# Kernel tuning notes

Measured on AMD Instinct MI355X. Metric: run time of the kernel, lower is better.

The kernel has to match this reference:

```python
import jax, jax.numpy as jnp
import numpy as np

B, T, C, H = 2, 2048, 1024, 16
HD = C // H  # head dim = 64


def setup_inputs() -> dict:
    key = jax.random.key(0)
    k1, k2, k3 = jax.random.split(key, 3)
    scale = 0.02
    x = jax.random.normal(k1, (B, T, C), dtype=jnp.float32)
    w_attn = jax.random.normal(k2, (C, 3 * C), dtype=jnp.float32) * scale
    b_attn = jnp.zeros((3 * C,), dtype=jnp.float32)
    w_proj = jax.random.normal(k3, (C, C), dtype=jnp.float32) * scale
    b_proj = jnp.zeros((C,), dtype=jnp.float32)
    return {"x": x, "w_attn": w_attn, "b_attn": b_attn, "w_proj": w_proj, "b_proj": b_proj}


def reference(x, w_attn, b_attn, w_proj, b_proj):
    b, t, c = x.shape
    qkv = x @ w_attn + b_attn  # [B,T,3C]
    q, k, v = jnp.split(qkv, 3, axis=-1)
    # [B,T,C] -> [B,H,T,HD]
    q = q.reshape(b, t, H, HD).transpose(0, 2, 1, 3)
    k = k.reshape(b, t, H, HD).transpose(0, 2, 1, 3)
    v = v.reshape(b, t, H, HD).transpose(0, 2, 1, 3)
    att = jnp.einsum('bhqd,bhkd->bhqk', q, k) * (1.0 / jnp.sqrt(jnp.float32(HD)))
    causal = jnp.tril(jnp.ones((t, t), dtype=bool))  # [T,T]
    att = jnp.where(causal[None, None, :, :], att, jnp.float32(-jnp.inf))
    att = jax.nn.softmax(att, axis=-1)
    y = jnp.einsum('bhqk,bhkd->bhqd', att, v)
    y = y.transpose(0, 2, 1, 3).reshape(b, t, c)
    return y @ w_proj + b_proj
```

## Files before the change

kernel.cpp:

```cpp
#include <hip/hip_runtime.h>


typedef unsigned short u16;
typedef unsigned short u16x8 __attribute__((ext_vector_type(8)));
typedef __bf16 bf16x8 __attribute__((ext_vector_type(8)));
typedef __bf16 bf16x4 __attribute__((ext_vector_type(4)));
typedef float f32x4 __attribute__((ext_vector_type(4)));

#define MFMA16(a, b, c) __builtin_amdgcn_mfma_f32_16x16x32_bf16(a, b, c, 0, 0, 0)

static __device__ __forceinline__ u16 f2b(float f) {
  union { float f; unsigned int i; } x; x.f = f;
  unsigned int r = x.i + 0x7fffu + ((x.i >> 16) & 1u);
  return (u16)(r >> 16);
}

static __device__ __forceinline__ void gload_lds16(const u16* g, u16* l) {
#if defined(__HIP_DEVICE_COMPILE__)
  __builtin_amdgcn_global_load_lds(
      (const __attribute__((address_space(1))) unsigned int*)g,
      (__attribute__((address_space(3))) unsigned int*)l,
      16, 0, 0);
#else
  (void)g; (void)l;
#endif
}

__global__ __launch_bounds__(256) void cast_f32_bf16(
    const float* __restrict__ in, u16* __restrict__ out) {
  int i = (blockIdx.x * 256 + threadIdx.x) * 8;
  float4 a = *(const float4*)&in[i];
  float4 b = *(const float4*)&in[i + 4];
  u16x8 o;
  o[0] = f2b(a.x); o[1] = f2b(a.y); o[2] = f2b(a.z); o[3] = f2b(a.w);
  o[4] = f2b(b.x); o[5] = f2b(b.y); o[6] = f2b(b.z); o[7] = f2b(b.w);
  *(u16x8*)&out[i] = o;
}

__global__ __launch_bounds__(256) void transpose_f32_bf16(
    const float* __restrict__ in, u16* __restrict__ out, int R, int Cc) {
  __shared__ u16 tile[32][33];
  int bx = blockIdx.x, by = blockIdx.y;
  int tx = threadIdx.x, ty = threadIdx.y;
#pragma unroll
  for (int i = 0; i < 4; i++) {
    int r = by * 32 + ty + i * 8;
    int c = bx * 32 + tx;
    tile[ty + i * 8][tx] = f2b(in[r * Cc + c]);
  }
  __syncthreads();
#pragma unroll
  for (int i = 0; i < 4; i++) {
    int r = bx * 32 + ty + i * 8;
    int c = by * 32 + tx;
    out[r * R + c] = tile[tx][ty + i * 8];
  }
}

__global__ __launch_bounds__(256) void transpose_v(
    const u16* __restrict__ in, u16* __restrict__ out) {
  int bh = blockIdx.y;
  int t = blockIdx.x * 128 + (threadIdx.x & 127);
  int dg = (threadIdx.x >> 7) * 32;
  const u16* src = in + (bh * 2048 + t) * 64;
  u16* dst = out + bh * 64 * 2048 + t;
#pragma unroll
  for (int i = 0; i < 32; i++) {
    int d = dg + i;
    dst[d * 2048] = src[d];
  }
}

template <int MODE>
__global__ __launch_bounds__(256, 2) void gemm_bt(
    const u16* __restrict__ A, const u16* __restrict__ Bt,
    const float* __restrict__ bias, float* __restrict__ out,
    u16* __restrict__ Qb, u16* __restrict__ Kb, u16* __restrict__ Vb,
    int M, int N, int K) {
  __shared__ u16 lA[128 * 32];
  __shared__ u16 lB[128 * 32];

  const int tid = threadIdx.x;
  const int lane = tid & 63;
  const int w = tid >> 6;
  const int wm = (w >> 1) * 64, wn = (w & 1) * 64;
  const int l15 = lane & 15, quad = lane >> 4;
  const int m0 = blockIdx.y * 128, n0 = blockIdx.x * 128;

  const int srow = lane >> 2;
  const int scol = (lane & 3) * 8;

  f32x4 acc[4][4] = {};

  for (int k0 = 0; k0 < K; k0 += 32) {
    __syncthreads();
#pragma unroll
    for (int h = 0; h < 2; h++) {
      int r = h * 64 + w * 16 + srow;
      gload_lds16(&A[(m0 + r) * K + k0 + scol], &lA[h * 2048 + w * 512 + lane * 8]);
      gload_lds16(&Bt[(n0 + r) * K + k0 + scol], &lB[h * 2048 + w * 512 + lane * 8]);
    }
    __syncthreads();

    bf16x8 af[4], bfr[4];
#pragma unroll
    for (int mi = 0; mi < 4; mi++)
      af[mi] = *(const bf16x8*)&lA[(wm + mi * 16 + l15) * 32 + quad * 8];
#pragma unroll
    for (int ni = 0; ni < 4; ni++)
      bfr[ni] = *(const bf16x8*)&lB[(wn + ni * 16 + l15) * 32 + quad * 8];
#pragma unroll
    for (int mi = 0; mi < 4; mi++)
#pragma unroll
      for (int ni = 0; ni < 4; ni++)
        acc[mi][ni] = MFMA16(af[mi], bfr[ni], acc[mi][ni]);
  }

#pragma unroll
  for (int mi = 0; mi < 4; mi++) {
#pragma unroll
    for (int ni = 0; ni < 4; ni++) {
      int n = n0 + wn + ni * 16 + l15;
      float bv = bias[n];
#pragma unroll
      for (int reg = 0; reg < 4; reg++) {
        int m = m0 + wm + mi * 16 + quad * 4 + reg;
        float v = acc[mi][ni][reg] + bv;
        if (MODE == 1) {
          out[m * N + n] = v;
        } else {
          int which = n >> 10;
          if (which == 1) v *= 0.18033688011112042f;
          int hn = n & 1023;
          int hh = hn >> 6, d = hn & 63;
          int b = m >> 11, t = m & 2047;
          u16* dst = (which == 0) ? Qb : ((which == 1) ? Kb : Vb);
          dst[(((b << 4) + hh) * 2048 + t) * 64 + d] = f2b(v);
        }
      }
    }
  }
}

__global__ __launch_bounds__(256, 4) void attn_kernel(
    const u16* __restrict__ Qg, const u16* __restrict__ Kg,
    const u16* __restrict__ Vt, u16* __restrict__ Yg) {
  __shared__ u16 lk[64 * 72];
  __shared__ u16 lvt[64 * 72];

  const int qt = 31 - blockIdx.x;
  const int bh = blockIdx.y;
  const int tid = threadIdx.x;
  const int lane = tid & 63;
  const int w = tid >> 6;
  const int l15 = lane & 15, quad = lane >> 4;
  const int qbase = qt * 64;
  const int base = bh * 2048 * 64;
  const int vbase = bh * 64 * 2048;

  const int sr = tid >> 3;
  const int sc = (tid & 7) * 8;

  const u16* qrow = Qg + base + (qbase + w * 16 + l15) * 64;
  bf16x8 bq0 = *(const bf16x8*)&qrow[quad * 8];
  bf16x8 bq1 = *(const bf16x8*)&qrow[32 + quad * 8];

  const u16* kp = Kg + base;
  const u16* vp = Vt + vbase;

  u16x8 kr[2], vr[2];
#pragma unroll
  for (int h = 0; h < 2; h++) {
    int r = sr + h * 32;
    kr[h] = *(const u16x8*)&kp[r * 64 + sc];
    vr[h] = *(const u16x8*)&vp[r * 2048 + sc];
  }

  f32x4 oacc[4] = {};
  float ls = 0.f;

  for (int kt = 0; kt <= qt; kt++) {
    __syncthreads();
#pragma unroll
    for (int h = 0; h < 2; h++) {
      int r = sr + h * 32;
      *(u16x8*)&lk[r * 72 + sc] = kr[h];
      *(u16x8*)&lvt[r * 72 + sc] = vr[h];
    }
    __syncthreads();
    if (kt < qt) {
      int kvb = (kt + 1) * 64;
#pragma unroll
      for (int h = 0; h < 2; h++) {
        int r = sr + h * 32;
        kr[h] = *(const u16x8*)&kp[(kvb + r) * 64 + sc];
        vr[h] = *(const u16x8*)&vp[r * 2048 + kvb + sc];
      }
    }

    const bool diag = (kt == qt);
    const int qloc = w * 16 + l15;

#pragma unroll
    for (int u = 0; u < 2; u++) {
      bf16x8 pa;
      float psum = 0.f;
#pragma unroll
      for (int half = 0; half < 2; half++) {
        int nt = 2 * u + half;
        bf16x8 ak0 = *(const bf16x8*)&lk[(nt * 16 + l15) * 72 + quad * 8];
        bf16x8 ak1 = *(const bf16x8*)&lk[(nt * 16 + l15) * 72 + 32 + quad * 8];
        f32x4 st = {};
        st = MFMA16(ak0, bq0, st);
        st = MFMA16(ak1, bq1, st);
#pragma unroll
        for (int reg = 0; reg < 4; reg++) {
          float s = st[reg];
          if (diag && (nt * 16 + quad * 4 + reg) > qloc) s = -1e30f;
          float p = exp2f(s);
          psum += p;
          pa[half * 4 + reg] = (__bf16)p;
        }
      }
      ls += psum;

#pragma unroll
      for (int dt = 0; dt < 4; dt++) {
        const u16* vrow = &lvt[(dt * 16 + l15) * 72 + u * 32 + quad * 4];
        bf16x4 lo = *(const bf16x4*)&vrow[0];
        bf16x4 hi = *(const bf16x4*)&vrow[16];
        bf16x8 bv;
#pragma unroll
        for (int j = 0; j < 4; j++) { bv[j] = lo[j]; bv[4 + j] = hi[j]; }
        oacc[dt] = MFMA16(pa, bv, oacc[dt]);
      }
    }
  }

  ls += __shfl_xor(ls, 16, 64);
  ls += __shfl_xor(ls, 32, 64);

  const int b = bh >> 4, hh = bh & 15;
  float inv[4];
#pragma unroll
  for (int reg = 0; reg < 4; reg++)
    inv[reg] = 1.0f / __shfl(ls, quad * 4 + reg, 64);
#pragma unroll
  for (int dt = 0; dt < 4; dt++)
#pragma unroll
    for (int reg = 0; reg < 4; reg++) {
      int q = qbase + w * 16 + quad * 4 + reg;
      int col = hh * 64 + dt * 16 + l15;
      Yg[(b * 2048 + q) * 1024 + col] = f2b(oacc[dt][reg] * inv[reg]);
    }
}

extern "C" void kernel_launch(void* const* d_in, const int* in_sizes, int n_in,
                              void* d_out, int out_size, void* d_ws, size_t ws_size,
                              hipStream_t stream) {
  const float* x      = (const float*)d_in[0];
  const float* w_attn = (const float*)d_in[1];
  const float* b_attn = (const float*)d_in[2];
  const float* w_proj = (const float*)d_in[3];
  const float* b_proj = (const float*)d_in[4];
  float* out = (float*)d_out;

  char* ws = (char*)d_ws;
  u16* wattnT = (u16*)(ws);
  u16* wprojT = (u16*)(ws + 6291456);
  u16* xb     = (u16*)(ws + 8388608);
  u16* Vt     = xb;
  u16* Qb     = (u16*)(ws + 16777216);
  u16* Kb     = (u16*)(ws + 25165824);
  u16* Vb     = (u16*)(ws + 33554432);
  u16* Yb     = (u16*)(ws + 41943040);

  cast_f32_bf16<<<2048, 256, 0, stream>>>(x, xb);
  transpose_f32_bf16<<<dim3(96, 32), dim3(32, 8), 0, stream>>>(w_attn, wattnT, 1024, 3072);
  transpose_f32_bf16<<<dim3(32, 32), dim3(32, 8), 0, stream>>>(w_proj, wprojT, 1024, 1024);
  gemm_bt<0><<<dim3(24, 32), 256, 0, stream>>>(xb, wattnT, b_attn, nullptr,
                                               Qb, Kb, Vb, 4096, 3072, 1024);
  transpose_v<<<dim3(16, 32), 256, 0, stream>>>(Vb, Vt);
  attn_kernel<<<dim3(32, 32), 256, 0, stream>>>(Qb, Kb, Vt, Yb);
  gemm_bt<1><<<dim3(8, 32), 256, 0, stream>>>(Yb, wprojT, b_proj, out,
                                              nullptr, nullptr, nullptr, 4096, 1024, 1024);
}
```

Measured before the change: 217.2 us.

## Split causal attention along the KV axis with a combine pass

Causal attention work per query tile is uneven, so the attention kernel is split into KV chunks of 8 tiles. Long query tiles get up to four blocks, and their unnormalized partial outputs and row sums are written to workspace. A small combine kernel then sums the partials and normalizes them. Row sums are now computed with an MFMA against a vector of ones instead of scalar adds and shuffles. The trade-off is an extra launch, partial outputs stored in bf16, and the split path only runs when the workspace is large enough.

After: 200.3 us. 7.8% less time.

```diff
diff --git a/kernel.cpp b/kernel.cpp
--- a/kernel.cpp
+++ b/kernel.cpp
@@ -13,6 +13,9 @@
   union { float f; unsigned int i; } x; x.f = f;
   unsigned int r = x.i + 0x7fffu + ((x.i >> 16) & 1u);
   return (u16)(r >> 16);
+}
+static __device__ __forceinline__ float b2f(u16 u) {
+  union { unsigned int i; float f; } x; x.i = ((unsigned int)u) << 16; return x.f;
 }
 
 static __device__ __forceinline__ void gload_lds16(const u16* g, u16* l) {
@@ -142,6 +145,175 @@
   }
 }
 
+__global__ __launch_bounds__(256, 4) void attn_split(
+    const u16* __restrict__ Qg, const u16* __restrict__ Kg,
+    const u16* __restrict__ Vt, u16* __restrict__ Yg,
+    u16* __restrict__ Opart, float* __restrict__ lpart) {
+  __shared__ u16 lk[64 * 72];
+  __shared__ u16 lvt[64 * 72];
+
+  const int x = blockIdx.x;
+  const int bh = blockIdx.y;
+  int qt, s, ns;
+  if (x < 8)       { qt = x;                s = 0;            ns = 1; }
+  else if (x < 24) { int r = x - 8;  qt = 8  + (r >> 1); s = r & 1; ns = 2; }
+  else if (x < 48) { int r = x - 24; qt = 16 + r / 3;    s = r % 3; ns = 3; }
+  else             { int r = x - 48; qt = 24 + (r >> 2); s = r & 3; ns = 4; }
+  const int kts = s * 8;
+  const int kend = (kts + 8 < qt + 1) ? (kts + 8) : (qt + 1);
+
+  const int tid = threadIdx.x;
+  const int lane = tid & 63;
+  const int w = tid >> 6;
+  const int l15 = lane & 15, quad = lane >> 4;
+  const int qbase = qt * 64;
+  const int base = bh * 2048 * 64;
+  const int vbase = bh * 64 * 2048;
+
+  const int sr = tid >> 3;
+  const int sc = (tid & 7) * 8;
+
+  const u16* qrow = Qg + base + (qbase + w * 16 + l15) * 64;
+  bf16x8 bq0 = *(const bf16x8*)&qrow[quad * 8];
+  bf16x8 bq1 = *(const bf16x8*)&qrow[32 + quad * 8];
+
+  u16x8 onesu = {0x3F80, 0x3F80, 0x3F80, 0x3F80, 0x3F80, 0x3F80, 0x3F80, 0x3F80};
+  bf16x8 ones = *(const bf16x8*)&onesu;
+
+  const u16* kp = Kg + base;
+  const u16* vp = Vt + vbase;
+
+  u16x8 kr[2], vr[2];
+  {
+    int kvb = kts * 64;
+#pragma unroll
+    for (int h = 0; h < 2; h++) {
+      int r = sr + h * 32;
+      kr[h] = *(const u16x8*)&kp[(kvb + r) * 64 + sc];
+      vr[h] = *(const u16x8*)&vp[r * 2048 + kvb + sc];
+    }
+  }
+
+  f32x4 oacc[4] = {};
+  f32x4 lacc = {};
+
+  for (int kt = kts; kt < kend; kt++) {
+    __syncthreads();
+#pragma unroll
+    for (int h = 0; h < 2; h++) {
+      int r = sr + h * 32;
+      *(u16x8*)&lk[r * 72 + sc] = kr[h];
+      *(u16x8*)&lvt[r * 72 + sc] = vr[h];
+    }
+    __syncthreads();
+    if (kt + 1 < kend) {
+      int kvb = (kt + 1) * 64;
+#pragma unroll
+      for (int h = 0; h < 2; h++) {
+        int r = sr + h * 32;
+        kr[h] = *(const u16x8*)&kp[(kvb + r) * 64 + sc];
+        vr[h] = *(const u16x8*)&vp[r * 2048 + kvb + sc];
+      }
+    }
+
+    const bool diag = (kt == qt);
+    const int qloc = w * 16 + l15;
+
+#pragma unroll
+    for (int u = 0; u < 2; u++) {
+      bf16x8 pa;
+#pragma unroll
+      for (int half = 0; half < 2; half++) {
+        int nt = 2 * u + half;
+        bf16x8 ak0 = *(const bf16x8*)&lk[(nt * 16 + l15) * 72 + quad * 8];
+        bf16x8 ak1 = *(const bf16x8*)&lk[(nt * 16 + l15) * 72 + 32 + quad * 8];
+        f32x4 st = {};
+        st = MFMA16(ak0, bq0, st);
+        st = MFMA16(ak1, bq1, st);
+#pragma unroll
+        for (int reg = 0; reg < 4; reg++) {
+          float sv = st[reg];
+          if (diag && (nt * 16 + quad * 4 + reg) > qloc) sv = -1e30f;
+          pa[half * 4 + reg] = (__bf16)exp2f(sv);
+        }
+      }
+      lacc = MFMA16(pa, ones, lacc);
+#pragma unroll
+      for (int dt = 0; dt < 4; dt++) {
+        const u16* vrow = &lvt[(dt * 16 + l15) * 72 + u * 32 + quad * 4];
+        bf16x4 lo = *(const bf16x4*)&vrow[0];
+        bf16x4 hi = *(const bf16x4*)&vrow[16];
+        bf16x8 bv;
+#pragma unroll
+        for (int j = 0; j < 4; j++) { bv[j] = lo[j]; bv[4 + j] = hi[j]; }
+        oacc[dt] = MFMA16(pa, bv, oacc[dt]);
+      }
+    }
+  }
+
+  if (ns == 1) {
+    const int b = bh >> 4, hh = bh & 15;
+    float inv[4];
+#pragma unroll
+    for (int reg = 0; reg < 4; reg++) inv[reg] = 1.0f / lacc[reg];
+#pragma unroll
+    for (int dt = 0; dt < 4; dt++)
+#pragma unroll
+      for (int reg = 0; reg < 4; reg++) {
+        int q = qbase + w * 16 + quad * 4 + reg;
+        int col = hh * 64 + dt * 16 + l15;
+        Yg[(b * 2048 + q) * 1024 + col] = f2b(oacc[dt][reg] * inv[reg]);
+      }
+  } else {
+    const int p = bh * 80 + x;
+    u16* op = Opart + p * 4096 + (w * 16) * 64;
+#pragma unroll
+    for (int dt = 0; dt < 4; dt++)
+#pragma unroll
+      for (int reg = 0; reg < 4; reg++)
+        op[(quad * 4 + reg) * 64 + dt * 16 + l15] = f2b(oacc[dt][reg]);
+    if (l15 == 0) {
+#pragma unroll
+      for (int reg = 0; reg < 4; reg++)
+        lpart[p * 64 + w * 16 + quad * 4 + reg] = lacc[reg];
+    }
+  }
+}
+
+__global__ __launch_bounds__(256) void attn_combine(
+    const u16* __restrict__ Opart, const float* __restrict__ lpart,
+    u16* __restrict__ Yg) {
+  const int qt = 8 + blockIdx.x;
+  const int bh = blockIdx.y;
+  const int tid = threadIdx.x;
+  const int row = tid >> 2;
+  const int cg = (tid & 3) * 16;
+  int xb, ns;
+  if (qt < 16)      { xb = 8  + (qt - 8) * 2;  ns = 2; }
+  else if (qt < 24) { xb = 24 + (qt - 16) * 3; ns = 3; }
+  else              { xb = 48 + (qt - 24) * 4; ns = 4; }
+
+  float acc[16] = {};
+  float lsum = 0.f;
+  for (int i = 0; i < ns; i++) {
+    int p = bh * 80 + xb + i;
+    lsum += lpart[p * 64 + row];
+    const u16* oprow = Opart + p * 4096 + row * 64 + cg;
+    u16x8 a = *(const u16x8*)&oprow[0];
+    u16x8 b = *(const u16x8*)&oprow[8];
+#pragma unroll
+    for (int j = 0; j < 8; j++) { acc[j] += b2f(a[j]); acc[8 + j] += b2f(b[j]); }
+  }
+  float inv = 1.0f / lsum;
+  u16x8 o0, o1;
+#pragma unroll
+  for (int j = 0; j < 8; j++) { o0[j] = f2b(acc[j] * inv); o1[j] = f2b(acc[8 + j] * inv); }
+  const int b = bh >> 4, hh = bh & 15;
+  u16* y = Yg + ((long)(b * 2048 + qt * 64 + row)) * 1024 + hh * 64 + cg;
+  *(u16x8*)&y[0] = o0;
+  *(u16x8*)&y[8] = o1;
+}
+
 __global__ __launch_bounds__(256, 4) void attn_kernel(
     const u16* __restrict__ Qg, const u16* __restrict__ Kg,
     const u16* __restrict__ Vt, u16* __restrict__ Yg) {
@@ -157,13 +329,15 @@
   const int qbase = qt * 64;
   const int base = bh * 2048 * 64;
   const int vbase = bh * 64 * 2048;
-
   const int sr = tid >> 3;
   const int sc = (tid & 7) * 8;
 
   const u16* qrow = Qg + base + (qbase + w * 16 + l15) * 64;
   bf16x8 bq0 = *(const bf16x8*)&qrow[quad * 8];
   bf16x8 bq1 = *(const bf16x8*)&qrow[32 + quad * 8];
+
+  u16x8 onesu = {0x3F80, 0x3F80, 0x3F80, 0x3F80, 0x3F80, 0x3F80, 0x3F80, 0x3F80};
+  bf16x8 ones = *(const bf16x8*)&onesu;
 
   const u16* kp = Kg + base;
   const u16* vp = Vt + vbase;
@@ -177,7 +351,7 @@
   }
 
   f32x4 oacc[4] = {};
-  float ls = 0.f;
+  f32x4 lacc = {};
 
   for (int kt = 0; kt <= qt; kt++) {
     __syncthreads();
@@ -200,11 +374,9 @@
 
     const bool diag = (kt == qt);
     const int qloc = w * 16 + l15;
-
 #pragma unroll
     for (int u = 0; u < 2; u++) {
       bf16x8 pa;
-      float psum = 0.f;
 #pragma unroll
       for (int half = 0; half < 2; half++) {
         int nt = 2 * u + half;
@@ -215,15 +387,12 @@
         st = MFMA16(ak1, bq1, st);
 #pragma unroll
         for (int reg = 0; reg < 4; reg++) {
-          float s = st[reg];
-          if (diag && (nt * 16 + quad * 4 + reg) > qloc) s = -1e30f;
-          float p = exp2f(s);
-          psum += p;
-          pa[half * 4 + reg] = (__bf16)p;
+          float sv = st[reg];
+          if (diag && (nt * 16 + quad * 4 + reg) > qloc) sv = -1e30f;
+          pa[half * 4 + reg] = (__bf16)exp2f(sv);
         }
       }
-      ls += psum;
-
+      lacc = MFMA16(pa, ones, lacc);
 #pragma unroll
       for (int dt = 0; dt < 4; dt++) {
         const u16* vrow = &lvt[(dt * 16 + l15) * 72 + u * 32 + quad * 4];
@@ -237,14 +406,10 @@
     }
   }
 
-  ls += __shfl_xor(ls, 16, 64);
-  ls += __shfl_xor(ls, 32, 64);
-
   const int b = bh >> 4, hh = bh & 15;
   float inv[4];
 #pragma unroll
-  for (int reg = 0; reg < 4; reg++)
-    inv[reg] = 1.0f / __shfl(ls, quad * 4 + reg, 64);
+  for (int reg = 0; reg < 4; reg++) inv[reg] = 1.0f / lacc[reg];
 #pragma unroll
   for (int dt = 0; dt < 4; dt++)
 #pragma unroll
@@ -274,6 +439,10 @@
   u16* Kb     = (u16*)(ws + 25165824);
   u16* Vb     = (u16*)(ws + 33554432);
   u16* Yb     = (u16*)(ws + 41943040);
+  u16* Opart  = (u16*)(ws + 50331648);
+  float* lpart = (float*)(ws + 71303168);
+
+  const bool split = (ws_size >= 71958528ULL);
 
   cast_f32_bf16<<<2048, 256, 0, stream>>>(x, xb);
   transpose_f32_bf16<<<dim3(96, 32), dim3(32, 8), 0, stream>>>(w_attn, wattnT, 1024, 3072);
@@ -281,7 +450,12 @@
   gemm_bt<0><<<dim3(24, 32), 256, 0, stream>>>(xb, wattnT, b_attn, nullptr,
                                                Qb, Kb, Vb, 4096, 3072, 1024);
   transpose_v<<<dim3(16, 32), 256, 0, stream>>>(Vb, Vt);
-  attn_kernel<<<dim3(32, 32), 256, 0, stream>>>(Qb, Kb, Vt, Yb);
+  if (split) {
+    attn_split<<<dim3(80, 32), 256, 0, stream>>>(Qb, Kb, Vt, Yb, Opart, lpart);
+    attn_combine<<<dim3(24, 32), 256, 0, stream>>>(Opart, lpart, Yb);
+  } else {
+    attn_kernel<<<dim3(32, 32), 256, 0, stream>>>(Qb, Kb, Vt, Yb);
+  }
   gemm_bt<1><<<dim3(8, 32), 256, 0, stream>>>(Yb, wprojT, b_proj, out,
                                               nullptr, nullptr, nullptr, 4096, 1024, 1024);
 }
```
